# Performance work log

Hardware: AMD Instinct MI355X
Metric: run time of the kernel (lower is better)

## Reference

```python
import jax, jax.numpy as jnp
import numpy as np

B, S, D, H = 4, 2048, 768, 12
HD = D // H  # 64
NEG_INF = -1000000000.0


def setup_inputs() -> dict:
    key = jax.random.key(0)
    k1, k2, k3 = jax.random.split(key, 3)
    scale_in = 1.0 / np.sqrt(D)
    return {
        "x": jax.random.normal(k1, (B, S, D), dtype=jnp.float32),
        "W_qkv": jax.random.normal(k2, (D, 3 * D), dtype=jnp.float32) * scale_in,
        "b_qkv": jnp.zeros((3 * D,), dtype=jnp.float32),
        "W_o": jax.random.normal(k3, (D, D), dtype=jnp.float32) * scale_in,
        "b_o": jnp.zeros((D,), dtype=jnp.float32),
    }


def reference(x, W_qkv, b_qkv, W_o, b_o):
    # qkv projection: [B,S,3D]
    qkv = x @ W_qkv + b_qkv
    q, k, v = jnp.split(qkv, 3, axis=-1)
    # split heads -> [B,H,S,HD]
    q = q.reshape(B, S, H, HD).transpose(0, 2, 1, 3)
    k = k.reshape(B, S, H, HD).transpose(0, 2, 1, 3)
    v = v.reshape(B, S, H, HD).transpose(0, 2, 1, 3)
    # scores [B,H,S,S], scaled by sqrt(head_dim)
    attn = jnp.einsum("bhqd,bhkd->bhqk", q, k) / jnp.sqrt(jnp.float32(HD))
    # faithful (idiosyncratic) masking from the original module:
    # attn = attn * mask; attn = attn + NEG_INF * (1 - attn)
    mask = jnp.tril(jnp.ones((S, S), dtype=attn.dtype))  # [S,S]
    attn = attn * mask
    attn = attn + NEG_INF * (1.0 - attn)
    attn = jax.nn.softmax(attn, axis=-1)
    # dropout is identity in inference
    ctx = jnp.einsum("bhqk,bhkd->bhqd", attn, v)  # [B,H,S,HD]
    ctx = ctx.transpose(0, 2, 1, 3).reshape(B, S, D)
    return ctx @ W_o + b_o
```

## Files before the change

### kernel.cpp

```cpp
#include <hip/hip_runtime.h>
#include <cmath>
#include <cstdint>
#include <cstddef>

namespace {
constexpr int kB = 4;
constexpr int kS = 2048;
constexpr int kD = 768;
constexpr int kH = 12;
constexpr int kHD = 64;
constexpr int k3D = 3 * kD;
constexpr float kNeg = -1000000000.0f;
constexpr float kDelta = 0.25f;
}

__device__ __forceinline__ float mask_affine(float a) {
#pragma clang fp contract(off)
    const float u = 1.0f - a;
    return a + kNeg * u;
}

__device__ __forceinline__ short bf16rne_s(float f) {
    uint32_t u = __builtin_bit_cast(uint32_t, f);
    u += 0x7FFFu + ((u >> 16) & 1u);
    return (short)(u >> 16);
}
__device__ __forceinline__ float bf16tof(short h) {
    const uint32_t u = ((uint32_t)(unsigned short)h) << 16;
    return __builtin_bit_cast(float, u);
}

template <int BM, int BN, int BK, int TM, int TN>
__global__ __launch_bounds__(BM * BN / (TM * TN))
void gemm_bias_kernel(const float* __restrict__ A, const float* __restrict__ Bm,
                      const float* __restrict__ bias, float* __restrict__ C,
                      int M, int K, int ldb, int ldc)
{
    constexpr int THREADS = BM * BN / (TM * TN);
    constexpr int TX = BN / TN;
    constexpr int TY = THREADS / TX;
    static_assert(TX == 16 && TY * TM == BM, "geometry");
    constexpr int AF4 = BM * BK / (THREADS * 4);
    constexpr int BF4 = BK * BN / (THREADS * 4);
    constexpr int BSTR = BK * TN + 4;

    __shared__ float As[2][BK][BM + 4];
    __shared__ float Bs[2][TX][BSTR];

    const int tid = threadIdx.x;
    const int tx = tid % TX, ty = tid / TX;
    const int m0 = blockIdx.y * BM, n0 = blockIdx.x * BN;

    float4 pa[AF4], pb[BF4];
    auto load_tiles = [&](int k0) {
#pragma unroll
        for (int it = 0; it < AF4; ++it) {
            const int e = (tid + it * THREADS) * 4;
            const int row = e / BK, col = e % BK;
            pa[it] = *reinterpret_cast<const float4*>(
                &A[(size_t)(m0 + row) * K + (k0 + col)]);
        }
#pragma unroll
        for (int it = 0; it < BF4; ++it) {
            const int e = (tid + it * THREADS) * 4;
            const int row = e / BN, col = e % BN;
            pb[it] = *reinterpret_cast<const float4*>(
                &Bm[(size_t)(k0 + row) * ldb + (n0 + col)]);
        }
    };
    auto commit = [&](int buf) {
#pragma unroll
        for (int it = 0; it < AF4; ++it) {
            const int e = (tid + it * THREADS) * 4;
            const int row = e / BK, col = e % BK;
            As[buf][col + 0][row] = pa[it].x;
            As[buf][col + 1][row] = pa[it].y;
            As[buf][col + 2][row] = pa[it].z;
            As[buf][col + 3][row] = pa[it].w;
        }
#pragma unroll
        for (int it = 0; it < BF4; ++it) {
            const int e = (tid + it * THREADS) * 4;
            const int row = e / BN, col = e % BN;
            const int g = col / TN, off = col % TN;
            *reinterpret_cast<float4*>(&Bs[buf][g][row * TN + off]) = pb[it];
        }
    };

    float acc[TM][TN];
#pragma unroll
    for (int i = 0; i < TM; ++i)
#pragma unroll
        for (int j = 0; j < TN; ++j) acc[i][j] = 0.0f;

    load_tiles(0);
    commit(0);
    load_tiles(BK);
    __syncthreads();

    int cur = 0;
    for (int k0 = 0; k0 < K; k0 += BK) {
        const bool has_next = (k0 + BK < K);
        if (has_next) {
            commit(cur ^ 1);
            if (k0 + 2 * BK < K) load_tiles(k0 + 2 * BK);
        }
#pragma unroll
        for (int kk = 0; kk < BK; ++kk) {
            float a[TM], b[TN];
#pragma unroll
            for (int i = 0; i < TM; i += 4) {
                const float4 v = *reinterpret_cast<const float4*>(
                    &As[cur][kk][ty * TM + i]);
                a[i] = v.x; a[i + 1] = v.y; a[i + 2] = v.z; a[i + 3] = v.w;
            }
#pragma unroll
            for (int j = 0; j < TN; j += 4) {
                const float4 v = *reinterpret_cast<const float4*>(
                    &Bs[cur][tx][kk * TN + j]);
                b[j] = v.x; b[j + 1] = v.y; b[j + 2] = v.z; b[j + 3] = v.w;
            }
#pragma unroll
            for (int i = 0; i < TM; ++i)
#pragma unroll
                for (int j = 0; j < TN; ++j)
                    acc[i][j] = fmaf(a[i], b[j], acc[i][j]);
        }
        if (has_next) __syncthreads();
        cur ^= 1;
    }

#pragma unroll
    for (int i = 0; i < TM; ++i) {
        const int m = m0 + ty * TM + i;
#pragma unroll
        for (int j = 0; j < TN; ++j) {
            const int n = n0 + tx * TN + j;
            C[(size_t)m * ldc + n] = acc[i][j] + bias[n];
        }
    }
}

__global__ __launch_bounds__(256)
void gemm_mfma_kernel(const float* __restrict__ A, const float* __restrict__ Bm,
                      const float* __restrict__ bias, float* __restrict__ C,
                      int M, int K, int ldb, int ldc)
{
    using f32x4 = __attribute__((ext_vector_type(4))) float;
    using s16x8 = __attribute__((ext_vector_type(8))) short;
    constexpr int BM = 128, BN = 64, BK = 32;
    constexpr int AST = 40;

    __shared__ unsigned short Ah[2][BM][AST];
    __shared__ unsigned short Al[2][BM][AST];
    __shared__ unsigned short Bh[2][BN][AST];

    const int tid = threadIdx.x;
    const int wave = tid >> 6, lane = tid & 63;
    const int jq = lane & 15, hi = lane >> 4;
    const int m0 = blockIdx.y * BM, n0 = blockIdx.x * BN;

    float4 pa[4], pb[2];
    auto load_tiles = [&](int k0) {
#pragma unroll
        for (int it = 0; it < 4; ++it) {
            const int e = (tid + it * 256) * 4;
            const int row = e / BK, col = e % BK;
            pa[it] = *reinterpret_cast<const float4*>(
                &A[(size_t)(m0 + row) * K + (k0 + col)]);
        }
#pragma unroll
        for (int it = 0; it < 2; ++it) {
            const int e = (tid + it * 256) * 4;
            const int krow = e / BN, ncol = e % BN;
            pb[it] = *reinterpret_cast<const float4*>(
                &Bm[(size_t)(k0 + krow) * ldb + (n0 + ncol)]);
        }
    };
    auto commit = [&](int buf) {
#pragma unroll
        for (int it = 0; it < 4; ++it) {
            const int e = (tid + it * 256) * 4;
            const int row = e / BK, col = e % BK;
            const float v[4] = {pa[it].x, pa[it].y, pa[it].z, pa[it].w};
            ushort4 uh, ul;
            unsigned short* ph = &uh.x;
            unsigned short* pl = &ul.x;
#pragma unroll
            for (int r = 0; r < 4; ++r) {
                const short hb = bf16rne_s(v[r]);
                ph[r] = (unsigned short)hb;
                pl[r] = (unsigned short)bf16rne_s(v[r] - bf16tof(hb));
            }
            *reinterpret_cast<ushort4*>(&Ah[buf][row][col]) = uh;
            *reinterpret_cast<ushort4*>(&Al[buf][row][col]) = ul;
        }
#pragma unroll
        for (int it = 0; it < 2; ++it) {
            const int e = (tid + it * 256) * 4;
            const int krow = e / BN, ncol = e % BN;
            Bh[buf][ncol + 0][krow] = (unsigned short)bf16rne_s(pb[it].x);
            Bh[buf][ncol + 1][krow] = (unsigned short)bf16rne_s(pb[it].y);
            Bh[buf][ncol + 2][krow] = (unsigned short)bf16rne_s(pb[it].z);
            Bh[buf][ncol + 3][krow] = (unsigned short)bf16rne_s(pb[it].w);
        }
    };

    f32x4 acc[2][4];
#pragma unroll
    for (int i = 0; i < 2; ++i)
#pragma unroll
        for (int j = 0; j < 4; ++j) acc[i][j] = {0.f, 0.f, 0.f, 0.f};

    load_tiles(0);
    commit(0);
    load_tiles(BK);
    __syncthreads();

    int cur = 0;
    for (int k0 = 0; k0 < K; k0 += BK) {
        const bool has_next = (k0 + BK < K);
        if (has_next) {
            commit(cur ^ 1);
            if (k0 + 2 * BK < K) load_tiles(k0 + 2 * BK);
        }
        s16x8 ahf[2], alf[2], bhf[4];
#pragma unroll
        for (int i = 0; i < 2; ++i) {
            ahf[i] = *reinterpret_cast<const s16x8*>(
                &Ah[cur][wave * 32 + i * 16 + jq][hi * 8]);
            alf[i] = *reinterpret_cast<const s16x8*>(
                &Al[cur][wave * 32 + i * 16 + jq][hi * 8]);
        }
#pragma unroll
        for (int j = 0; j < 4; ++j)
            bhf[j] = *reinterpret_cast<const s16x8*>(
                &Bh[cur][j * 16 + jq][hi * 8]);
#pragma unroll
        for (int i = 0; i < 2; ++i)
#pragma unroll
            for (int j = 0; j < 4; ++j) {
                f32x4 c = acc[i][j];
                c = __builtin_amdgcn_mfma_f32_16x16x32_bf16(ahf[i], bhf[j], c, 0, 0, 0);
                c = __builtin_amdgcn_mfma_f32_16x16x32_bf16(alf[i], bhf[j], c, 0, 0, 0);
                acc[i][j] = c;
            }
        if (has_next) __syncthreads();
        cur ^= 1;
    }

#pragma unroll
    for (int i = 0; i < 2; ++i) {
        const int mbase = m0 + wave * 32 + i * 16 + hi * 4;
#pragma unroll
        for (int j = 0; j < 4; ++j) {
            const int n = n0 + j * 16 + jq;
            const float bv = bias[n];
#pragma unroll
            for (int r = 0; r < 4; ++r)
                C[(size_t)(mbase + r) * ldc + n] = acc[i][j][r] + bv;
        }
    }
}

__global__ __launch_bounds__(256)
void vsuf_kernel(const float* __restrict__ qkv, float* __restrict__ vsuf)
{
    const int h = blockIdx.x, b = blockIdx.y;
    const int lane = threadIdx.x & 63, wave = threadIdx.x >> 6;
    const float* vp = qkv + (size_t)b * kS * k3D + 2 * kD + h * kHD;
    float* op = vsuf + (size_t)(b * kH + h) * kS * kHD;
    __shared__ float csum[4][64];

    const int kBeg = wave * 512, kEnd = kBeg + 512;
    float s = 0.0f;
#pragma unroll 8
    for (int k = kBeg; k < kEnd; ++k)
        s += vp[(size_t)k * k3D + lane];
    csum[wave][lane] = s;
    __syncthreads();

    float run = 0.0f;
    for (int w = wave + 1; w < 4; ++w) run += csum[w][lane];
#pragma unroll 8
    for (int k = kEnd - 1; k >= kBeg; --k) {
        run += vp[(size_t)k * k3D + lane];
        op[(size_t)k * kHD + lane] = run;
    }
}

__global__ __launch_bounds__(256, 3)
void attn_mfma_kernel(const float* __restrict__ qkv,
                      const float* __restrict__ vsuf,
                      float* __restrict__ ctx)
{
    using f32x4 = __attribute__((ext_vector_type(4))) float;
    using s16x8 = __attribute__((ext_vector_type(8))) short;

    const int id = blockIdx.x;
    const int bh = id % (kB * kH);
    const int t  = id / (kB * kH);
    const int b = bh / kH, h = bh % kH;

    const int tid = threadIdx.x;
    const int wave = tid >> 6, lane = tid & 63;
    const int jq = lane & 15, hi = lane >> 4;
    const int qrow = wave * 16 + jq;
    const int qglob = t * 64 + qrow;

    __shared__ float Qf[64][68];
    __shared__ float Kf[64][68];
    __shared__ unsigned short Kb[64][72];
    __shared__ float Msh[64];
    __shared__ float MgS[64];
    __shared__ int   CgS[64], I0S[64], I1S[64];

    const float* qp = qkv + (size_t)b * kS * k3D + h * kHD;
    const float* kp = qp + kD;
    const float* vp = qp + 2 * kD;

#pragma unroll
    for (int i = 0; i < 4; ++i) {
        const int f4 = tid + i * 256;
        const int r = f4 >> 4, d4 = f4 & 15;
        float4 v = *reinterpret_cast<const float4*>(
            &qp[(size_t)(t * 64 + r) * k3D + d4 * 4]);
        v.x *= 0.125f; v.y *= 0.125f; v.z *= 0.125f; v.w *= 0.125f;
        *reinterpret_cast<float4*>(&Qf[r][d4 * 4]) = v;
    }
    __syncthreads();

    auto mkfrag = [&](const float* p) {
        const float4 a = *reinterpret_cast<const float4*>(p);
        const float4 c = *reinterpret_cast<const float4*>(p + 4);
        s16x8 r;
        r[0] = bf16rne_s(a.x); r[1] = bf16rne_s(a.y);
        r[2] = bf16rne_s(a.z); r[3] = bf16rne_s(a.w);
        r[4] = bf16rne_s(c.x); r[5] = bf16rne_s(c.y);
        r[6] = bf16rne_s(c.z); r[7] = bf16rne_s(c.w);
        return r;
    };

    const s16x8 bq0 = mkfrag(&Qf[qrow][hi * 8]);
    const s16x8 bq1 = mkfrag(&Qf[qrow][32 + hi * 8]);

    auto stage_kb = [&](int kt) {
#pragma unroll
        for (int i = 0; i < 4; ++i) {
            const int f4 = tid + i * 256;
            const int r = f4 >> 4, d4 = f4 & 15;
            const float4 v = *reinterpret_cast<const float4*>(
                &kp[(size_t)(kt * 64 + r) * k3D + d4 * 4]);
            ushort4 u;
            u.x = (unsigned short)bf16rne_s(v.x);
            u.y = (unsigned short)bf16rne_s(v.y);
            u.z = (unsigned short)bf16rne_s(v.z);
            u.w = (unsigned short)bf16rne_s(v.w);
            *reinterpret_cast<ushort4*>(&Kb[r][d4 * 4]) = u;
        }
    };
    auto stage_both = [&](int kt) {
#pragma unroll
        for (int i = 0; i < 4; ++i) {
            const int f4 = tid + i * 256;
            const int r = f4 >> 4, d4 = f4 & 15;
            const float4 v = *reinterpret_cast<const float4*>(
                &kp[(size_t)(kt * 64 + r) * k3D + d4 * 4]);
            *reinterpret_cast<float4*>(&Kf[r][d4 * 4]) = v;
            ushort4 u;
            u.x = (unsigned short)bf16rne_s(v.x);
            u.y = (unsigned short)bf16rne_s(v.y);
            u.z = (unsigned short)bf16rne_s(v.z);
            u.w = (unsigned short)bf16rne_s(v.w);
            *reinterpret_cast<ushort4*>(&Kb[r][d4 * 4]) = u;
        }
    };

    auto score_tile = [&](f32x4* acc) {
#pragma unroll
        for (int g = 0; g < 4; ++g) {
            const s16x8 a0 = *reinterpret_cast<const s16x8*>(
                &Kb[g * 16 + jq][hi * 8]);
            const s16x8 a1 = *reinterpret_cast<const s16x8*>(
                &Kb[g * 16 + jq][32 + hi * 8]);
            f32x4 c = {0.f, 0.f, 0.f, 0.f};
            c = __builtin_amdgcn_mfma_f32_16x16x32_bf16(a0, bq0, c, 0, 0, 0);
            c = __builtin_amdgcn_mfma_f32_16x16x32_bf16(a1, bq1, c, 0, 0, 0);
            acc[g] = c;
        }
    };

    float mt = -INFINITY;
    for (int kt = 0; kt <= t; ++kt) {
        __syncthreads();
        stage_kb(kt);
        __syncthreads();
        f32x4 acc[4];
        score_tile(acc);
#pragma unroll
        for (int g = 0; g < 4; ++g)
#pragma unroll
            for (int r = 0; r < 4; ++r) {
                const int key = kt * 64 + g * 16 + hi * 4 + r;
                if (key <= qglob) mt = fmaxf(mt, acc[g][r]);
            }
    }
    mt = fmaxf(mt, __shfl_xor(mt, 16));
    mt = fmaxf(mt, __shfl_xor(mt, 32));
    if (hi == 0) Msh[wave * 16 + jq] = mt;
    __syncthreads();
    const float thr = Msh[wave * 16 + jq] - kDelta;

    float m = -INFINITY;
    int cnt = 0, i0 = -1, i1 = -1;
    for (int kt = 0; kt <= t; ++kt) {
        __syncthreads();
        stage_both(kt);
        __syncthreads();
        f32x4 acc[4];
        score_tile(acc);
#pragma unroll
        for (int g = 0; g < 4; ++g)
#pragma unroll
            for (int r = 0; r < 4; ++r) {
                const int key = kt * 64 + g * 16 + hi * 4 + r;
                if (key <= qglob && acc[g][r] > thr) {
                    const float* qr = &Qf[qrow][0];
                    const float* kr = &Kf[key - kt * 64][0];
                    float dot = 0.0f;
#pragma unroll
                    for (int d4 = 0; d4 < 16; ++d4) {
                        const float4 q4 = *reinterpret_cast<const float4*>(qr + d4 * 4);
                        const float4 k4 = *reinterpret_cast<const float4*>(kr + d4 * 4);
                        dot = fmaf(q4.x, k4.x, dot);
                        dot = fmaf(q4.y, k4.y, dot);
                        dot = fmaf(q4.z, k4.z, dot);
                        dot = fmaf(q4.w, k4.w, dot);
                    }
                    const float s = mask_affine(dot);
                    const bool upd = (s > m), tie = (s == m);
                    i1 = upd ? -1 : ((tie && cnt == 1) ? key : i1);
                    i0 = upd ? key : i0;
                    cnt = upd ? 1 : (tie ? cnt + 1 : cnt);
                    m = upd ? s : m;
                }
            }
    }

#pragma unroll
    for (int off = 16; off <= 32; off <<= 1) {
        const float mo = __shfl_xor(m, off);
        const int co = __shfl_xor(cnt, off);
        const int o0 = __shfl_xor(i0, off);
        const int o1 = __shfl_xor(i1, off);
        if (mo > m) { m = mo; cnt = co; i0 = o0; i1 = o1; }
        else if (mo == m && co > 0) {
            if (cnt == 0) { i0 = o0; i1 = o1; }
            else if (cnt == 1) { i1 = o0; }
            cnt += co;
        }
    }
    if (hi == 0) {
        MgS[wave * 16 + jq] = m; CgS[wave * 16 + jq] = cnt;
        I0S[wave * 16 + jq] = i0; I1S[wave * 16 + jq] = i1;
    }
    __syncthreads();

    const int qloc = tid >> 2, qtr = tid & 3;
    const int qi = t * 64 + qloc;
    float mg = MgS[qloc];
    int fcnt = CgS[qloc], f0 = I0S[qloc], f1 = I1S[qloc];

    bool addsuf = false;
    if (qi < kS - 1) {
        const bool lt = (mg < kNeg), eq = (mg == kNeg);
        if (lt)      { fcnt = kS - 1 - qi; f0 = -1; f1 = -1; addsuf = true; }
        else if (eq) { fcnt += kS - 1 - qi; addsuf = true; }
    }

    float4 a4[4];
#pragma unroll
    for (int i = 0; i < 4; ++i) a4[i] = {0.f, 0.f, 0.f, 0.f};

    if (f0 >= 0) {
        const float* vr = vp + (size_t)f0 * k3D + qtr * 16;
#pragma unroll
        for (int i = 0; i < 4; ++i) {
            const float4 v = *reinterpret_cast<const float4*>(vr + i * 4);
            a4[i].x += v.x; a4[i].y += v.y; a4[i].z += v.z; a4[i].w += v.w;
        }
    }
    if (f1 >= 0) {
        const float* vr = vp + (size_t)f1 * k3D + qtr * 16;
#pragma unroll
        for (int i = 0; i < 4; ++i) {
            const float4 v = *reinterpret_cast<const float4*>(vr + i * 4);
            a4[i].x += v.x; a4[i].y += v.y; a4[i].z += v.z; a4[i].w += v.w;
        }
    }
    if (addsuf) {
        const float* sp = vsuf + ((size_t)(b * kH + h) * kS + (qi + 1)) * kHD
                          + qtr * 16;
#pragma unroll
        for (int i = 0; i < 4; ++i) {
            const float4 v = *reinterpret_cast<const float4*>(sp + i * 4);
            a4[i].x += v.x; a4[i].y += v.y; a4[i].z += v.z; a4[i].w += v.w;
        }
    }

    float* op = ctx + ((size_t)b * kS + qi) * kD + h * kHD + qtr * 16;
    const float fc = (float)fcnt;
#pragma unroll
    for (int i = 0; i < 4; ++i) {
        const float4 r = {a4[i].x / fc, a4[i].y / fc, a4[i].z / fc, a4[i].w / fc};
        *reinterpret_cast<float4*>(op + i * 4) = r;
    }
}

extern "C" void kernel_launch(void* const* d_in, const int* in_sizes, int n_in,
                              void* d_out, int out_size, void* d_ws, size_t ws_size,
                              hipStream_t stream)
{
    const float* x     = (const float*)d_in[0];
    const float* W_qkv = (const float*)d_in[1];
    const float* b_qkv = (const float*)d_in[2];
    const float* W_o   = (const float*)d_in[3];
    const float* b_o   = (const float*)d_in[4];
    float* out = (float*)d_out;

    float* qkv  = (float*)d_ws;
    float* ctx  = qkv + (size_t)kB * kS * k3D;
    float* vsuf = out;

    {
        dim3 grid(1536 / 128, (kB * kS) / 128);
        gemm_bias_kernel<128, 128, 16, 8, 8><<<grid, 256, 0, stream>>>(
            x, W_qkv, b_qkv, qkv, kB * kS, kD, k3D, k3D);
    }
    {
        dim3 grid(kD / 64, (kB * kS) / 128);
        gemm_mfma_kernel<<<grid, 256, 0, stream>>>(
            x, W_qkv + 2 * kD, b_qkv + 2 * kD, qkv + 2 * kD,
            kB * kS, kD, k3D, k3D);
    }
    {
        dim3 grid(kH, kB);
        vsuf_kernel<<<grid, 256, 0, stream>>>(qkv, vsuf);
    }
    {
        attn_mfma_kernel<<<dim3((kS / 64) * kB * kH), 256, 0, stream>>>(
            qkv, vsuf, ctx);
    }
    {
        dim3 grid(kD / 64, (kB * kS) / 128);
        gemm_mfma_kernel<<<grid, 256, 0, stream>>>(
            ctx, W_o, b_o, out, kB * kS, kD, kD, kD);
    }
}
```

Measured before the change: 575.8 us.

## Transpose A-tile staging via lane shuffles and swizzle QKV GEMM blocks across XCDs

The fp32 QKV GEMM used to write its A tile into transposed shared memory as four scalar stores per float4. It now runs a 4x4 transpose across lanes with two rounds of xor shuffles, so each thread writes one float4 row segment, cutting LDS store instructions and bank conflicts. The launch also switches to a 1D grid with an XCD-aware swizzle, so blocks sharing the same M rows land on the same XCD for better L2 reuse. The cost is extra shuffle instructions, and the swizzle assumes M/BM divides evenly by 8.

After: 576.3 us. About the same (+0.1%).

```diff
diff --git a/kernel.cpp b/kernel.cpp
--- a/kernel.cpp
+++ b/kernel.cpp
@@ -30,7 +30,7 @@
     return __builtin_bit_cast(float, u);
 }
 
-template <int BM, int BN, int BK, int TM, int TN>
+template <int BM, int BN, int BK, int TM, int TN, bool SWZ>
 __global__ __launch_bounds__(BM * BN / (TM * TN))
 void gemm_bias_kernel(const float* __restrict__ A, const float* __restrict__ Bm,
                       const float* __restrict__ bias, float* __restrict__ C,
@@ -40,6 +40,7 @@
     constexpr int TX = BN / TN;
     constexpr int TY = THREADS / TX;
     static_assert(TX == 16 && TY * TM == BM, "geometry");
+    static_assert(BK == 16 && THREADS == 256, "transpose-staging mapping");
     constexpr int AF4 = BM * BK / (THREADS * 4);
     constexpr int BF4 = BK * BN / (THREADS * 4);
     constexpr int BSTR = BK * TN + 4;
@@ -49,7 +50,20 @@
 
     const int tid = threadIdx.x;
     const int tx = tid % TX, ty = tid / TX;
-    const int m0 = blockIdx.y * BM, n0 = blockIdx.x * BN;
+
+    int bxs, bys;
+    if (SWZ) {
+        const int nby = M / BM;
+        const int per = nby >> 3;
+        const int id = blockIdx.x;
+        const int xcd = id & 7, i2 = id >> 3;
+        bxs = i2 / per;
+        bys = xcd * per + (i2 % per);
+    } else {
+        bxs = blockIdx.x;
+        bys = blockIdx.y;
+    }
+    const int m0 = bys * BM, n0 = bxs * BN;
 
     float4 pa[AF4], pb[BF4];
     auto load_tiles = [&](int k0) {
@@ -72,11 +86,29 @@
 #pragma unroll
         for (int it = 0; it < AF4; ++it) {
             const int e = (tid + it * THREADS) * 4;
-            const int row = e / BK, col = e % BK;
-            As[buf][col + 0][row] = pa[it].x;
-            As[buf][col + 1][row] = pa[it].y;
-            As[buf][col + 2][row] = pa[it].z;
-            As[buf][col + 3][row] = pa[it].w;
+            const int row = e / BK;
+            const int col = e % BK;
+            const int j = (tid >> 2) & 3;
+            float v0 = pa[it].x, v1 = pa[it].y, v2 = pa[it].z, v3 = pa[it].w;
+            {
+                const bool odd = (j & 1) != 0;
+                float s0 = odd ? v0 : v1;
+                float s1 = odd ? v2 : v3;
+                s0 = __shfl_xor(s0, 4);
+                s1 = __shfl_xor(s1, 4);
+                if (odd) { v0 = s0; v2 = s1; } else { v1 = s0; v3 = s1; }
+            }
+            {
+                const bool hi2 = (j & 2) != 0;
+                float s0 = hi2 ? v0 : v2;
+                float s1 = hi2 ? v1 : v3;
+                s0 = __shfl_xor(s0, 8);
+                s1 = __shfl_xor(s1, 8);
+                if (hi2) { v0 = s0; v1 = s1; } else { v2 = s0; v3 = s1; }
+            }
+            const int r0 = row & ~3;
+            const float4 w = {v0, v1, v2, v3};
+            *reinterpret_cast<float4*>(&As[buf][col + j][r0]) = w;
         }
 #pragma unroll
         for (int it = 0; it < BF4; ++it) {
@@ -533,8 +565,7 @@
     float* vsuf = out;
 
     {
-        dim3 grid(1536 / 128, (kB * kS) / 128);
-        gemm_bias_kernel<128, 128, 16, 8, 8><<<grid, 256, 0, stream>>>(
+        gemm_bias_kernel<128, 128, 16, 8, 8, true><<<dim3(768), 256, 0, stream>>>(
             x, W_qkv, b_qkv, qkv, kB * kS, kD, k3D, k3D);
     }
     {
```

## Compute Q/K projection with 3-way bf16-split MFMA instead of FP32 SIMT GEMM

Applied to the files above, without the earlier changes.

Replaces the FP32 SIMT GEMM for the Q and K columns of the QKV projection with a bf16 MFMA GEMM. The operands are pre-split into three bf16 terms (high, mid, low) and combined with eight cross-product MFMAs to keep near-FP32 accuracy. Two extra kernels split x and transpose-split W_qkv into workspace, which adds memory traffic and launches. The path runs only if the workspace is large enough, otherwise it falls back to the old kernel.

Measured after the change: 476.5 us, median of 2. -17.2%, faster.

```diff
diff --git a/kernel.cpp b/kernel.cpp
--- a/kernel.cpp
+++ b/kernel.cpp
@@ -12,6 +12,15 @@
 constexpr int k3D = 3 * kD;
 constexpr float kNeg = -1000000000.0f;
 constexpr float kDelta = 0.25f;
+constexpr int kNQK = 1536;
+
+constexpr size_t kOfsQkv = 0;
+constexpr size_t kOfsCtx = (size_t)kB * kS * k3D * 4;
+constexpr size_t kOfsXh  = kOfsCtx + (size_t)kB * kS * kD * 4;
+constexpr size_t kSzX    = (size_t)kB * kS * kD * 2;
+constexpr size_t kOfsWh  = kOfsXh + 3 * kSzX;
+constexpr size_t kSzW    = (size_t)kD * kNQK * 2;
+constexpr size_t kNeedWs = kOfsWh + 3 * kSzW;
 }
 
 __device__ __forceinline__ float mask_affine(float a) {
@@ -28,6 +37,16 @@
 __device__ __forceinline__ float bf16tof(short h) {
     const uint32_t u = ((uint32_t)(unsigned short)h) << 16;
     return __builtin_bit_cast(float, u);
+}
+__device__ __forceinline__ void split3(float v, unsigned short& h,
+                                       unsigned short& m, unsigned short& l) {
+    const short hs = bf16rne_s(v);
+    const float r1 = v - bf16tof(hs);
+    const short ms = bf16rne_s(r1);
+    const float r2 = r1 - bf16tof(ms);
+    h = (unsigned short)hs;
+    m = (unsigned short)ms;
+    l = (unsigned short)bf16rne_s(r2);
 }
 
 template <int BM, int BN, int BK, int TM, int TN>
@@ -137,6 +156,152 @@
         for (int j = 0; j < TN; ++j) {
             const int n = n0 + tx * TN + j;
             C[(size_t)m * ldc + n] = acc[i][j] + bias[n];
+        }
+    }
+}
+
+__global__ __launch_bounds__(256)
+void split_x_kernel(const float* __restrict__ x, unsigned short* __restrict__ xh,
+                    unsigned short* __restrict__ xm, unsigned short* __restrict__ xl)
+{
+    const size_t total4 = (size_t)kB * kS * kD / 4;
+    for (size_t i4 = blockIdx.x * 256 + threadIdx.x; i4 < total4;
+         i4 += (size_t)gridDim.x * 256) {
+        const float4 v = *reinterpret_cast<const float4*>(&x[i4 * 4]);
+        ushort4 h, m, l;
+        split3(v.x, h.x, m.x, l.x);
+        split3(v.y, h.y, m.y, l.y);
+        split3(v.z, h.z, m.z, l.z);
+        split3(v.w, h.w, m.w, l.w);
+        *reinterpret_cast<ushort4*>(&xh[i4 * 4]) = h;
+        *reinterpret_cast<ushort4*>(&xm[i4 * 4]) = m;
+        *reinterpret_cast<ushort4*>(&xl[i4 * 4]) = l;
+    }
+}
+
+__global__ __launch_bounds__(256)
+void split_w_kernel(const float* __restrict__ W,
+                    unsigned short* __restrict__ Wh,
+                    unsigned short* __restrict__ Wm,
+                    unsigned short* __restrict__ Wl)
+{
+    __shared__ unsigned short Th[64][72], Tm[64][72], Tl[64][72];
+    const int k0 = blockIdx.x * 64, n0 = blockIdx.y * 64;
+    const int tid = threadIdx.x;
+
+#pragma unroll
+    for (int i = 0; i < 16; ++i) {
+        const int idx = tid + i * 256;
+        const int kk = idx >> 6, nn = idx & 63;
+        const float v = W[(size_t)(k0 + kk) * k3D + (n0 + nn)];
+        split3(v, Th[nn][kk], Tm[nn][kk], Tl[nn][kk]);
+    }
+    __syncthreads();
+#pragma unroll
+    for (int i = 0; i < 16; ++i) {
+        const int idx = tid + i * 256;
+        const int nn = idx >> 6, kk = idx & 63;
+        const size_t o = (size_t)(n0 + nn) * kD + (k0 + kk);
+        Wh[o] = Th[nn][kk];
+        Wm[o] = Tm[nn][kk];
+        Wl[o] = Tl[nn][kk];
+    }
+}
+
+__global__ __launch_bounds__(256)
+void qk_mfma_kernel(const unsigned short* __restrict__ xh,
+                    const unsigned short* __restrict__ xm,
+                    const unsigned short* __restrict__ xl,
+                    const unsigned short* __restrict__ Wh,
+                    const unsigned short* __restrict__ Wm,
+                    const unsigned short* __restrict__ Wl,
+                    const float* __restrict__ bias, float* __restrict__ C)
+{
+    using f32x4 = __attribute__((ext_vector_type(4))) float;
+    using s16x8 = __attribute__((ext_vector_type(8))) short;
+
+    __shared__ unsigned short Axs[3][128][40];
+    __shared__ unsigned short Bxs[3][64][40];
+
+    const int tid = threadIdx.x;
+    const int wave = tid >> 6, lane = tid & 63;
+    const int jq = lane & 15, hi = lane >> 4;
+    const int n0 = blockIdx.x * 64, m0 = blockIdx.y * 128;
+
+    const unsigned short* Xs[3] = {xh, xm, xl};
+    const unsigned short* Ws[3] = {Wh, Wm, Wl};
+
+    f32x4 acc[2][4];
+#pragma unroll
+    for (int i = 0; i < 2; ++i)
+#pragma unroll
+        for (int j = 0; j < 4; ++j) acc[i][j] = {0.f, 0.f, 0.f, 0.f};
+
+    for (int kt = 0; kt < kD / 32; ++kt) {
+        const int k0 = kt * 32;
+        __syncthreads();
+#pragma unroll
+        for (int s = 0; s < 3; ++s) {
+#pragma unroll
+            for (int it = 0; it < 4; ++it) {
+                const int e = (tid + it * 256) * 4;
+                const int row = e >> 5, col = e & 31;
+                *reinterpret_cast<ushort4*>(&Axs[s][row][col]) =
+                    *reinterpret_cast<const ushort4*>(
+                        &Xs[s][(size_t)(m0 + row) * kD + (k0 + col)]);
+            }
+#pragma unroll
+            for (int it = 0; it < 2; ++it) {
+                const int e = (tid + it * 256) * 4;
+                const int row = e >> 5, col = e & 31;
+                *reinterpret_cast<ushort4*>(&Bxs[s][row][col]) =
+                    *reinterpret_cast<const ushort4*>(
+                        &Ws[s][(size_t)(n0 + row) * kD + (k0 + col)]);
+            }
+        }
+        __syncthreads();
+
+        s16x8 af[2][3];
+#pragma unroll
+        for (int i = 0; i < 2; ++i)
+#pragma unroll
+            for (int s = 0; s < 3; ++s)
+                af[i][s] = *reinterpret_cast<const s16x8*>(
+                    &Axs[s][wave * 32 + i * 16 + jq][hi * 8]);
+
+#pragma unroll
+        for (int j = 0; j < 4; ++j) {
+            s16x8 bf[3];
+#pragma unroll
+            for (int s = 0; s < 3; ++s)
+                bf[s] = *reinterpret_cast<const s16x8*>(
+                    &Bxs[s][j * 16 + jq][hi * 8]);
+#pragma unroll
+            for (int i = 0; i < 2; ++i) {
+                f32x4 c = acc[i][j];
+                c = __builtin_amdgcn_mfma_f32_16x16x32_bf16(af[i][0], bf[0], c, 0, 0, 0);
+                c = __builtin_amdgcn_mfma_f32_16x16x32_bf16(af[i][1], bf[0], c, 0, 0, 0);
+                c = __builtin_amdgcn_mfma_f32_16x16x32_bf16(af[i][0], bf[1], c, 0, 0, 0);
+                c = __builtin_amdgcn_mfma_f32_16x16x32_bf16(af[i][2], bf[0], c, 0, 0, 0);
+                c = __builtin_amdgcn_mfma_f32_16x16x32_bf16(af[i][1], bf[1], c, 0, 0, 0);
+                c = __builtin_amdgcn_mfma_f32_16x16x32_bf16(af[i][0], bf[2], c, 0, 0, 0);
+                c = __builtin_amdgcn_mfma_f32_16x16x32_bf16(af[i][2], bf[1], c, 0, 0, 0);
+                c = __builtin_amdgcn_mfma_f32_16x16x32_bf16(af[i][1], bf[2], c, 0, 0, 0);
+                acc[i][j] = c;
+            }
+        }
+    }
+
+#pragma unroll
+    for (int i = 0; i < 2; ++i) {
+        const int mbase = m0 + wave * 32 + i * 16 + hi * 4;
+#pragma unroll
+        for (int j = 0; j < 4; ++j) {
+            const int n = n0 + j * 16 + jq;
+            const float bv = bias[n];
+#pragma unroll
+            for (int r = 0; r < 4; ++r)
+                C[(size_t)(mbase + r) * k3D + n] = acc[i][j][r] + bv;
         }
     }
 }
@@ -528,12 +693,26 @@
     const float* b_o   = (const float*)d_in[4];
     float* out = (float*)d_out;
 
-    float* qkv  = (float*)d_ws;
-    float* ctx  = qkv + (size_t)kB * kS * k3D;
+    char* ws = (char*)d_ws;
+    float* qkv  = (float*)(ws + kOfsQkv);
+    float* ctx  = (float*)(ws + kOfsCtx);
     float* vsuf = out;
 
-    {
-        dim3 grid(1536 / 128, (kB * kS) / 128);
+    if (ws_size >= kNeedWs) {
+        unsigned short* xh = (unsigned short*)(ws + kOfsXh);
+        unsigned short* xm = xh + (size_t)kB * kS * kD;
+        unsigned short* xl = xm + (size_t)kB * kS * kD;
+        unsigned short* Wh = (unsigned short*)(ws + kOfsWh);
+        unsigned short* Wm = Wh + (size_t)kD * kNQK;
+        unsigned short* Wl = Wm + (size_t)kD * kNQK;
+
+        split_x_kernel<<<dim3(1024), 256, 0, stream>>>(x, xh, xm, xl);
+        split_w_kernel<<<dim3(kD / 64, kNQK / 64), 256, 0, stream>>>(
+            W_qkv, Wh, Wm, Wl);
+        qk_mfma_kernel<<<dim3(kNQK / 64, (kB * kS) / 128), 256, 0, stream>>>(
+            xh, xm, xl, Wh, Wm, Wl, b_qkv, qkv);
+    } else {
+        dim3 grid(kNQK / 128, (kB * kS) / 128);
         gemm_bias_kernel<128, 128, 16, 8, 8><<<grid, 256, 0, stream>>>(
             x, W_qkv, b_qkv, qkv, kB * kS, kD, k3D, k3D);
     }
```
